# Kernel optimization log

Hardware: AMD Instinct MI355X
Metric: run time of the kernel (lower is better)

Reference implementation:

```python
import jax, jax.numpy as jnp
import numpy as np

EPS = 1e-5

def conv3(x, w, b):
    # 3x3 conv, stride 1, pad 1, NCHW/OIHW
    y = jax.lax.conv_general_dilated(x, w, (1, 1), ((1, 1), (1, 1)),
                                     dimension_numbers=('NCHW', 'OIHW', 'NCHW'))
    return y + b[None, :, None, None]

def positional_norm(x):
    # per-pixel channel-wise norm; torch .var() is unbiased (ddof=1)
    mean = jnp.mean(x, axis=1, keepdims=True)
    var = jnp.var(x, axis=1, keepdims=True, ddof=1)
    return (x - mean) / jnp.sqrt(var + EPS)

def bilinear_gather(x, py, px):
    # x: [B,C,H,W]; py/px: [B,K,H,W] absolute sample coords -> [B,C,K,H,W]
    B, C, H, W = x.shape
    K = py.shape[1]
    xf = x.reshape(B, C, H * W)
    y0 = jnp.floor(py).astype(jnp.int32)
    x0 = jnp.floor(px).astype(jnp.int32)
    wy = py - y0.astype(x.dtype)
    wx = px - x0.astype(x.dtype)

    def corner(yi, xi):
        valid = ((yi >= 0) & (yi < H) & (xi >= 0) & (xi < W)).astype(x.dtype)
        idx = (jnp.clip(yi, 0, H - 1) * W + jnp.clip(xi, 0, W - 1)).reshape(B, 1, K * H * W)
        v = jnp.take_along_axis(xf, idx, axis=2).reshape(B, C, K, H, W)
        return v * valid[:, None]

    out = ((1 - wy) * (1 - wx))[:, None] * corner(y0, x0)
    out = out + ((1 - wy) * wx)[:, None] * corner(y0, x0 + 1)
    out = out + (wy * (1 - wx))[:, None] * corner(y0 + 1, x0)
    out = out + (wy * wx)[:, None] * corner(y0 + 1, x0 + 1)
    return out

def dcn_v2(feat, cond, w_off, b_off, w_dcn, b_dcn):
    # DCNv2Pack: conv_offset(cond) -> (o1, o2, mask); modulated deformable 3x3 conv on feat
    B, C, H, W = feat.shape
    om = conv3(cond, w_off, b_off)                      # [B, 27, H, W]
    off = om[:, :18].reshape(B, 9, 2, H, W)             # (dy, dx) per kernel tap
    mask = jax.nn.sigmoid(om[:, 18:])                   # [B, 9, H, W]
    dy, dx = off[:, :, 0], off[:, :, 1]
    ki = jnp.repeat(jnp.arange(-1.0, 2.0, dtype=feat.dtype), 3)   # tap row offsets
    kj = jnp.tile(jnp.arange(-1.0, 2.0, dtype=feat.dtype), 3)     # tap col offsets
    hh = jnp.arange(H, dtype=feat.dtype)
    ww = jnp.arange(W, dtype=feat.dtype)
    py = dy + hh[None, None, :, None] + ki[None, :, None, None]
    px = dx + ww[None, None, None, :] + kj[None, :, None, None]
    sampled = bilinear_gather(feat, py, px)             # [B,C,9,H,W]
    wk = w_dcn.reshape(w_dcn.shape[0], C, 9)
    out = jnp.einsum('bkhw,bckhw,ock->bohw', mask, sampled, wk)
    return out + b_dcn[None, :, None, None]

def spade_forward(x, ref, w1, b1, w2, b2, w_off, b_off, w_dcn, b_dcn, w_g, b_g, w_be, b_be):
    normalized = positional_norm(x)
    h = jax.nn.relu(conv3(jnp.concatenate((normalized, ref), axis=1), w1, b1))
    cond = jax.nn.relu(conv3(h, w2, b2))
    ref_refine = dcn_v2(ref, cond, w_off, b_off, w_dcn, b_dcn)
    gamma = conv3(ref_refine, w_g, b_g)
    beta = conv3(ref_refine, w_be, b_be)
    return normalized * (1 + gamma) + beta

def setup_inputs() -> dict:
    key = jax.random.key(0)
    ks = jax.random.split(key, 16)
    B, NC, SC, H, W = 2, 64, 64, 96, 96
    mid = (NC + SC) // 8  # 16
    s = 0.05
    inp = {
        'x': jax.random.normal(ks[0], (B, NC, H, W), jnp.float32),
        'ref': jax.random.normal(ks[1], (B, SC, H, W), jnp.float32),
        'w1': jax.random.normal(ks[2], (mid, NC + SC, 3, 3), jnp.float32) * s,
        'b1': jax.random.normal(ks[3], (mid,), jnp.float32) * s,
        'w2': jax.random.normal(ks[4], (SC, mid, 3, 3), jnp.float32) * s,
        'b2': jax.random.normal(ks[5], (SC,), jnp.float32) * s,
        'w_off': jax.random.normal(ks[6], (27, SC, 3, 3), jnp.float32) * 0.01,
        'b_off': jax.random.normal(ks[7], (27,), jnp.float32) * 0.01,
        'w_dcn': jax.random.normal(ks[8], (SC, SC, 3, 3), jnp.float32) * s,
        'b_dcn': jax.random.normal(ks[9], (SC,), jnp.float32) * s,
        'w_g': jax.random.normal(ks[10], (NC, SC, 3, 3), jnp.float32) * s,
        'b_g': jax.random.normal(ks[11], (NC,), jnp.float32) * s,
        'w_be': jax.random.normal(ks[12], (NC, SC, 3, 3), jnp.float32) * s,
        'b_be': jax.random.normal(ks[13], (NC,), jnp.float32) * s,
    }
    return inp

def reference(x, ref, w1, b1, w2, b2, w_off, b_off, w_dcn, b_dcn, w_g, b_g, w_be, b_be):
    return spade_forward(x, ref, w1, b1, w2, b2, w_off, b_off, w_dcn, b_dcn, w_g, b_g, w_be, b_be)
```

## Files before the change

kernel.cpp:

```cpp
#include <hip/hip_runtime.h>
#include <math.h>

namespace {

typedef __attribute__((ext_vector_type(8))) short          bf16x8;
typedef __attribute__((ext_vector_type(8))) unsigned short u16x8;
typedef __attribute__((ext_vector_type(4))) float          f32x4;

constexpr int B_  = 2;
constexpr int H_  = 96;
constexpr int W_  = 96;
constexpr int HW_ = H_ * W_;
constexpr int NC_ = 64;
constexpr int SC_ = 64;

__device__ inline unsigned short f2bf(float f) {
    union { float f; unsigned u; } v; v.f = f;
    unsigned r = v.u + 0x7FFFu + ((v.u >> 16) & 1u);
    return (unsigned short)(r >> 16);
}
__device__ inline float bf2f(unsigned short s) {
    union { unsigned u; float f; } v; v.u = ((unsigned)s) << 16; return v.f;
}
__device__ inline bf16x8 ld_frag(const unsigned short* p) {
    return *reinterpret_cast<const bf16x8*>(p);
}

__global__ __launch_bounds__(256)
void prologue(const float* __restrict__ x, const float* __restrict__ ref,
              const float* __restrict__ w1, const float* __restrict__ w2,
              const float* __restrict__ woff, const float* __restrict__ wg,
              const float* __restrict__ wbe, const float* __restrict__ wdcn,
              float* __restrict__ nrm, unsigned short* __restrict__ cc,
              unsigned short* __restrict__ wt1, unsigned short* __restrict__ wt2,
              unsigned short* __restrict__ wtoff, unsigned short* __restrict__ wtg,
              unsigned short* __restrict__ wtbe, unsigned short* __restrict__ wbd) {
    __shared__ float red1[4][64];
    __shared__ float red2[4][64];
    __shared__ float rtile[64][65];

    int blk = blockIdx.x;
    int t   = threadIdx.x;

    if (blk < 288) {
        int b  = blk / 144;
        int p0 = (blk % 144) * 64;
        int px = t & 63;
        int cg = t >> 6;
        int p  = p0 + px;

        float v[16];
        float s1 = 0.f, s2 = 0.f;
        const float* xb = x + ((size_t)b * NC_ + cg * 16) * HW_ + p;
        #pragma unroll
        for (int j = 0; j < 16; ++j) {
            v[j] = xb[j * HW_];
            s1 += v[j];
            s2 = fmaf(v[j], v[j], s2);
        }
        red1[cg][px] = s1;
        red2[cg][px] = s2;

        const float* rb = ref + (size_t)b * SC_ * HW_ + p0 + px;
        #pragma unroll
        for (int it = 0; it < 16; ++it) {
            int ch = it * 4 + cg;
            rtile[ch][px] = rb[(size_t)ch * HW_];
        }
        __syncthreads();

        s1 = red1[0][px] + red1[1][px] + red1[2][px] + red1[3][px];
        s2 = red2[0][px] + red2[1][px] + red2[2][px] + red2[3][px];
        float mean = s1 * (1.f / 64.f);
        float var  = (s2 - 64.f * mean * mean) * (1.f / 63.f);
        float inv  = 1.f / sqrtf(var + 1e-5f);
        float* nb = nrm + ((size_t)b * NC_ + cg * 16) * HW_ + p;
        u16x8 pk[2];
        #pragma unroll
        for (int j = 0; j < 16; ++j) {
            float nv = (v[j] - mean) * inv;
            nb[j * HW_] = nv;
            pk[j >> 3][j & 7] = f2bf(nv);
        }
        size_t bp = (size_t)b * HW_ + p;
        *reinterpret_cast<u16x8*>(&cc[bp * 128 + cg * 16 + 0]) = pk[0];
        *reinterpret_cast<u16x8*>(&cc[bp * 128 + cg * 16 + 8]) = pk[1];

        {
            int wpx = t >> 2, q = t & 3;
            size_t bp2 = (size_t)b * HW_ + p0 + wpx;
            u16x8 o0, o1;
            #pragma unroll
            for (int j = 0; j < 8; ++j) {
                o0[j] = f2bf(rtile[q * 16 + j][wpx]);
                o1[j] = f2bf(rtile[q * 16 + 8 + j][wpx]);
            }
            *reinterpret_cast<u16x8*>(&cc[bp2 * 128 + 64 + q * 16 + 0]) = o0;
            *reinterpret_cast<u16x8*>(&cc[bp2 * 128 + 64 + q * 16 + 8]) = o1;
        }
    } else {
        int idx = (blk - 288) * 256 + t;
        if (idx < 9 * 16 * 128) {
            int tap = idx / (16 * 128), oc = (idx / 128) % 16, ic = idx % 128;
            wt1[idx] = f2bf(w1[(oc * 128 + ic) * 9 + tap]);
        }
        if (idx < 9 * 64 * 32) {
            int tap = idx / (64 * 32), oc = (idx / 32) % 64, ic = idx % 32;
            wt2[idx] = (ic < 16) ? f2bf(w2[(oc * 16 + ic) * 9 + tap]) : (unsigned short)0;
        }
        if (idx < 9 * 32 * 64) {
            int tap = idx / (32 * 64), oc = (idx / 64) % 32, ic = idx % 64;
            wtoff[idx] = (oc < 27) ? f2bf(woff[(oc * 64 + ic) * 9 + tap]) : (unsigned short)0;
        }
        if (idx < 9 * 64 * 64) {
            int tap = idx / (64 * 64), oc = (idx / 64) % 64, ic = idx % 64;
            wtg[idx]  = f2bf(wg [(oc * 64 + ic) * 9 + tap]);
            wtbe[idx] = f2bf(wbe[(oc * 64 + ic) * 9 + tap]);
        }
        if (idx < 64 * 576) {
            int oc = idx / 576, r = idx - oc * 576;
            int tap = r >> 6, ic = r & 63;
            wbd[idx] = f2bf(wdcn[oc * 576 + ic * 9 + tap]);
        }
    }
}

template <int ICS, int ICP, int COLP, int COUT_PAD, int COUT_REAL,
          bool DUAL, bool RELU, int OMODE>
__global__ __launch_bounds__(256)
void conv_bf(const unsigned short* __restrict__ in,
             const unsigned short* __restrict__ Wt,
             const unsigned short* __restrict__ Wt2,
             const float* __restrict__ bias, const float* __restrict__ bias2,
             const float* __restrict__ nrm, float* __restrict__ outF,
             unsigned short* __restrict__ outB) {
    constexpr int NOCT = COUT_PAD / 16;
    constexpr int WPO  = 4 / NOCT;
    constexpr int MTP  = NOCT;
    constexpr int NACC = DUAL ? 2 : 1;
    constexpr int NKS  = ICP / 32;
    constexpr int NCH8 = ICP / 8;

    __shared__ unsigned short patch[6 * 18 * COLP];

    int t   = threadIdx.x;
    int blk = blockIdx.x;
    int bx  = blk % 6;
    int by  = (blk / 6) % 24;
    int b   = blk / 144;
    int x0  = bx * 16, y0 = by * 4;

    for (int e = t; e < 6 * 18 * NCH8; e += 256) {
        int kc  = e % NCH8;
        int col = (e / NCH8) % 18;
        int row = e / (NCH8 * 18);
        int yy = y0 + row - 1, xx = x0 + col - 1;
        bf16x8 v = (bf16x8){0, 0, 0, 0, 0, 0, 0, 0};
        if (kc * 8 < ICS && (unsigned)yy < (unsigned)H_ && (unsigned)xx < (unsigned)W_) {
            v = ld_frag(&in[((size_t)b * HW_ + yy * W_ + xx) * ICS + kc * 8]);
        }
        *reinterpret_cast<bf16x8*>(&patch[(row * 18 + col) * COLP + kc * 8]) = v;
    }
    __syncthreads();

    int wave = t >> 6, lane = t & 63;
    int fr = lane & 15, fq = lane >> 4;
    int oct  = wave / WPO;
    int widx = wave - oct * WPO;
    int mt0  = widx * MTP;

    f32x4 acc[MTP][NACC];
    #pragma unroll
    for (int i = 0; i < MTP; ++i)
        #pragma unroll
        for (int a = 0; a < NACC; ++a)
            acc[i][a] = (f32x4){0.f, 0.f, 0.f, 0.f};

    constexpr int dyv[9] = {0,0,0,1,1,1,2,2,2};
    constexpr int dxv[9] = {0,1,2,0,1,2,0,1,2};

    #pragma unroll
    for (int tap = 0; tap < 9; ++tap) {
        int dy = dyv[tap], dx = dxv[tap];
        #pragma unroll
        for (int ks = 0; ks < NKS; ++ks) {
            const size_t wo = ((size_t)tap * COUT_PAD + oct * 16 + fr) * ICP + ks * 32 + fq * 8;
            bf16x8 wfA = ld_frag(&Wt[wo]);
            bf16x8 wfB;
            if (DUAL) wfB = ld_frag(&Wt2[wo]);
            #pragma unroll
            for (int i = 0; i < MTP; ++i) {
                bf16x8 pf = ld_frag(&patch[((mt0 + i + dy) * 18 + (fr + dx)) * COLP
                                           + ks * 32 + fq * 8]);
                acc[i][0] = __builtin_amdgcn_mfma_f32_16x16x32_bf16(wfA, pf, acc[i][0], 0, 0, 0);
                if (DUAL)
                    acc[i][1] = __builtin_amdgcn_mfma_f32_16x16x32_bf16(wfB, pf, acc[i][1], 0, 0, 0);
            }
        }
    }

    #pragma unroll
    for (int i = 0; i < MTP; ++i) {
        int py = mt0 + i;
        if (OMODE == 1) {
            size_t p = (size_t)b * HW_ + (size_t)(y0 + py) * W_ + x0 + fr;
            ushort4 sv;
            #pragma unroll
            for (int j = 0; j < 4; ++j) {
                float v = acc[i][0][j] + bias[oct * 16 + fq * 4 + j];
                if (RELU) v = fmaxf(v, 0.f);
                ((unsigned short*)&sv)[j] = f2bf(v);
            }
            *reinterpret_cast<ushort4*>(&outB[p * COUT_REAL + oct * 16 + fq * 4]) = sv;
        } else if (OMODE == 2) {
            size_t p = (size_t)b * HW_ + (size_t)(y0 + py) * W_ + x0 + fr;
            float4 o4;
            #pragma unroll
            for (int j = 0; j < 4; ++j) {
                int oc = oct * 16 + fq * 4 + j;
                float v = acc[i][0][j] + (oc < COUT_REAL ? bias[oc] : 0.f);
                ((float*)&o4)[j] = v;
            }
            *reinterpret_cast<float4*>(&outF[p * 32 + oct * 16 + fq * 4]) = o4;
        } else {
            #pragma unroll
            for (int j = 0; j < 4; ++j) {
                int oc = oct * 16 + fq * 4 + j;
                if (oc >= COUT_REAL) continue;
                size_t off = ((size_t)b * COUT_REAL + oc) * HW_
                           + (size_t)(y0 + py) * W_ + x0 + fr;
                float v = acc[i][0][j] + bias[oc];
                if (DUAL) {
                    float be = acc[i][1][j] + bias2[oc];
                    float nv = nrm[off];
                    outF[off] = fmaf(nv, 1.f + v, be);
                } else {
                    outF[off] = RELU ? fmaxf(v, 0.f) : v;
                }
            }
        }
    }
}

constexpr int SROW = 584;
constexpr int DT   = 32;

__global__ __launch_bounds__(256)
void dcn_kernel(const unsigned short* __restrict__ cc, const float* __restrict__ omP,
                const unsigned short* __restrict__ wbd, const float* __restrict__ b_dcn,
                unsigned short* __restrict__ rrT) {
    __shared__ unsigned short sS[DT * SROW];
    __shared__ float4 cwL[DT * 9];
    __shared__ int4   ciL[DT * 9];

    int t = threadIdx.x;
    int bid = blockIdx.x;
    int swz = (bid & 7) * 72 + (bid >> 3);
    int b   = swz / (HW_ / DT);
    int p0  = (swz % (HW_ / DT)) * DT;

    const unsigned short* ccb = cc + (size_t)b * HW_ * 128;

    for (int e = t; e < DT * 9; e += 256) {
        int pp = e / 9, k = e - pp * 9;
        int p  = p0 + pp;
        int y  = p / W_, x = p - y * W_;
        const float* omp = &omP[(size_t)(b * HW_ + p) * 32];
        float dy = omp[2 * k];
        float dx = omp[2 * k + 1];
        float mk = omp[18 + k];
        mk = 1.f / (1.f + expf(-mk));

        float py = dy + (float)y + (float)(k / 3 - 1);
        float px = dx + (float)x + (float)(k % 3 - 1);
        float fy = floorf(py), fx = floorf(px);
        int   y0 = (int)fy,   x0 = (int)fx;
        float wy = py - fy,   wx = px - fx;

        float cw[4];
        int   ci[4];
        #pragma unroll
        for (int i = 0; i < 4; ++i) {
            int yy = y0 + (i >> 1);
            int xx = x0 + (i & 1);
            bool valid = (yy >= 0) && (yy < H_) && (xx >= 0) && (xx < W_);
            int yc = yy < 0 ? 0 : (yy > H_ - 1 ? H_ - 1 : yy);
            int xc = xx < 0 ? 0 : (xx > W_ - 1 ? W_ - 1 : xx);
            ci[i] = yc * W_ + xc;
            float wyi = (i >> 1) ? wy : (1.f - wy);
            float wxi = (i & 1)  ? wx : (1.f - wx);
            cw[i] = valid ? mk * wyi * wxi : 0.f;
        }
        cwL[e] = make_float4(cw[0], cw[1], cw[2], cw[3]);
        ciL[e] = make_int4(ci[0], ci[1], ci[2], ci[3]);
    }
    __syncthreads();

    {
        int pp = t >> 3, cg8 = t & 7;
        #pragma unroll
        for (int k = 0; k < 9; ++k) {
            float4 cw = cwL[pp * 9 + k];
            int4   ci = ciL[pp * 9 + k];
            u16x8 r0 = *reinterpret_cast<const u16x8*>(&ccb[(size_t)ci.x * 128 + 64 + cg8 * 8]);
            u16x8 r1 = *reinterpret_cast<const u16x8*>(&ccb[(size_t)ci.y * 128 + 64 + cg8 * 8]);
            u16x8 r2 = *reinterpret_cast<const u16x8*>(&ccb[(size_t)ci.z * 128 + 64 + cg8 * 8]);
            u16x8 r3 = *reinterpret_cast<const u16x8*>(&ccb[(size_t)ci.w * 128 + 64 + cg8 * 8]);
            u16x8 sv;
            #pragma unroll
            for (int j = 0; j < 8; ++j) {
                float v = cw.x * bf2f(r0[j]) + cw.y * bf2f(r1[j])
                        + cw.z * bf2f(r2[j]) + cw.w * bf2f(r3[j]);
                sv[j] = f2bf(v);
            }
            *reinterpret_cast<u16x8*>(&sS[pp * SROW + k * 64 + cg8 * 8]) = sv;
        }
    }
    __syncthreads();

    int wave = t >> 6, lane = t & 63;
    int fr = lane & 15, fq = lane >> 4;

    f32x4 acc0 = (f32x4){0.f, 0.f, 0.f, 0.f};
    f32x4 acc1 = (f32x4){0.f, 0.f, 0.f, 0.f};
    for (int ks = 0; ks < 18; ++ks) {
        bf16x8 wf  = ld_frag(&wbd[(size_t)(wave * 16 + fr) * 576 + ks * 32 + fq * 8]);
        bf16x8 pf0 = ld_frag(&sS[(size_t)fr * SROW + ks * 32 + fq * 8]);
        bf16x8 pf1 = ld_frag(&sS[(size_t)(16 + fr) * SROW + ks * 32 + fq * 8]);
        acc0 = __builtin_amdgcn_mfma_f32_16x16x32_bf16(wf, pf0, acc0, 0, 0, 0);
        acc1 = __builtin_amdgcn_mfma_f32_16x16x32_bf16(wf, pf1, acc1, 0, 0, 0);
    }

    {
        size_t p = (size_t)b * HW_ + p0 + fr;
        ushort4 sv0, sv1;
        #pragma unroll
        for (int j = 0; j < 4; ++j) {
            float bo = b_dcn[wave * 16 + fq * 4 + j];
            ((unsigned short*)&sv0)[j] = f2bf(acc0[j] + bo);
            ((unsigned short*)&sv1)[j] = f2bf(acc1[j] + bo);
        }
        *reinterpret_cast<ushort4*>(&rrT[p * 64 + wave * 16 + fq * 4]) = sv0;
        *reinterpret_cast<ushort4*>(&rrT[(p + 16) * 64 + wave * 16 + fq * 4]) = sv1;
    }
}

}

extern "C" void kernel_launch(void* const* d_in, const int* in_sizes, int n_in,
                              void* d_out, int out_size, void* d_ws, size_t ws_size,
                              hipStream_t stream) {
    (void)in_sizes; (void)n_in; (void)out_size; (void)ws_size;

    const float* x     = (const float*)d_in[0];
    const float* ref   = (const float*)d_in[1];
    const float* w1    = (const float*)d_in[2];
    const float* b1    = (const float*)d_in[3];
    const float* w2    = (const float*)d_in[4];
    const float* b2    = (const float*)d_in[5];
    const float* w_off = (const float*)d_in[6];
    const float* b_off = (const float*)d_in[7];
    const float* w_dcn = (const float*)d_in[8];
    const float* b_dcn = (const float*)d_in[9];
    const float* w_g   = (const float*)d_in[10];
    const float* b_g   = (const float*)d_in[11];
    const float* w_be  = (const float*)d_in[12];
    const float* b_be  = (const float*)d_in[13];

    float* out = (float*)d_out;
    float* ws  = (float*)d_ws;

    float* nrm = ws;
    float* omP = nrm + 1179648;
    unsigned short* cc    = (unsigned short*)(omP + 589824);
    unsigned short* hmidT = cc    + 2359296;
    unsigned short* condT = hmidT + 294912;
    unsigned short* rrT   = condT + 1179648;
    unsigned short* wt1   = rrT   + 1179648;
    unsigned short* wt2   = wt1   + 18432;
    unsigned short* wtoff = wt2   + 18432;
    unsigned short* wtg   = wtoff + 18432;
    unsigned short* wtbe  = wtg   + 36864;
    unsigned short* wbd   = wtbe  + 36864;

    prologue<<<432, 256, 0, stream>>>(x, ref, w1, w2, w_off, w_g, w_be, w_dcn,
                                      nrm, cc, wt1, wt2, wtoff, wtg, wtbe, wbd);

    constexpr int GRID = 288;

    conv_bf<128, 128, 136, 16, 16, false, true, 1>
        <<<GRID, 256, 0, stream>>>(cc, wt1, nullptr, b1, nullptr, nullptr, nullptr, hmidT);

    conv_bf<16, 32, 40, 64, 64, false, true, 1>
        <<<GRID, 256, 0, stream>>>(hmidT, wt2, nullptr, b2, nullptr, nullptr, nullptr, condT);

    conv_bf<64, 64, 72, 32, 27, false, false, 2>
        <<<GRID, 256, 0, stream>>>(condT, wtoff, nullptr, b_off, nullptr, nullptr, omP, nullptr);

    dcn_kernel<<<B_ * (HW_ / DT), 256, 0, stream>>>(cc, omP, wbd, b_dcn, rrT);

    conv_bf<64, 64, 72, 64, 64, true, false, 0>
        <<<GRID, 256, 0, stream>>>(rrT, wtg, wtbe, b_g, b_be, nrm, out, nullptr);
}
```

Baseline: 68.44 us.

## Fuse offset conv into DCN kernel and switch bilinear sampling to fp16

The separate offset/mask conv launch and its fp32 workspace round trip are removed. Each DCN block now loads a 3x34 halo of condT into shared memory and computes its 27 offset channels with MFMA before sampling. The bilinear gather also reads a new compact fp16 copy of ref (64 channels per pixel instead of a 128-wide interleaved buffer), blends with packed fp16 math, and the DCN GEMM uses fp16 MFMA. This saves a launch and memory traffic but adds per-block conv work, extra prologue writes, and fp16 range/precision risk.

New measurement: 68.02 us. No clear change (-0.6%).

```diff
diff --git a/kernel.cpp b/kernel.cpp
--- a/kernel.cpp
+++ b/kernel.cpp
@@ -5,6 +5,7 @@
 
 typedef __attribute__((ext_vector_type(8))) short          bf16x8;
 typedef __attribute__((ext_vector_type(8))) unsigned short u16x8;
+typedef __attribute__((ext_vector_type(8))) _Float16       f16x8;
 typedef __attribute__((ext_vector_type(4))) float          f32x4;
 
 constexpr int B_  = 2;
@@ -19,8 +20,11 @@
     unsigned r = v.u + 0x7FFFu + ((v.u >> 16) & 1u);
     return (unsigned short)(r >> 16);
 }
-__device__ inline float bf2f(unsigned short s) {
-    union { unsigned u; float f; } v; v.u = ((unsigned)s) << 16; return v.f;
+__device__ inline unsigned short f2hbits(float f) {
+    union { _Float16 h; unsigned short u; } s; s.h = (_Float16)f; return s.u;
+}
+__device__ inline _Float16 hfrombits(unsigned short u) {
+    union { _Float16 h; unsigned short u; } s; s.u = u; return s.h;
 }
 __device__ inline bf16x8 ld_frag(const unsigned short* p) {
     return *reinterpret_cast<const bf16x8*>(p);
@@ -32,9 +36,10 @@
               const float* __restrict__ woff, const float* __restrict__ wg,
               const float* __restrict__ wbe, const float* __restrict__ wdcn,
               float* __restrict__ nrm, unsigned short* __restrict__ cc,
+              unsigned short* __restrict__ ccH,
               unsigned short* __restrict__ wt1, unsigned short* __restrict__ wt2,
               unsigned short* __restrict__ wtoff, unsigned short* __restrict__ wtg,
-              unsigned short* __restrict__ wtbe, unsigned short* __restrict__ wbd) {
+              unsigned short* __restrict__ wtbe, unsigned short* __restrict__ wbdH) {
     __shared__ float red1[4][64];
     __shared__ float red2[4][64];
     __shared__ float rtile[64][65];
@@ -89,14 +94,18 @@
         {
             int wpx = t >> 2, q = t & 3;
             size_t bp2 = (size_t)b * HW_ + p0 + wpx;
-            u16x8 o0, o1;
+            u16x8 o0, o1, h0, h1;
             #pragma unroll
             for (int j = 0; j < 8; ++j) {
-                o0[j] = f2bf(rtile[q * 16 + j][wpx]);
-                o1[j] = f2bf(rtile[q * 16 + 8 + j][wpx]);
+                float v0 = rtile[q * 16 + j][wpx];
+                float v1 = rtile[q * 16 + 8 + j][wpx];
+                o0[j] = f2bf(v0);    o1[j] = f2bf(v1);
+                h0[j] = f2hbits(v0); h1[j] = f2hbits(v1);
             }
             *reinterpret_cast<u16x8*>(&cc[bp2 * 128 + 64 + q * 16 + 0]) = o0;
             *reinterpret_cast<u16x8*>(&cc[bp2 * 128 + 64 + q * 16 + 8]) = o1;
+            *reinterpret_cast<u16x8*>(&ccH[bp2 * 64 + q * 16 + 0]) = h0;
+            *reinterpret_cast<u16x8*>(&ccH[bp2 * 64 + q * 16 + 8]) = h1;
         }
     } else {
         int idx = (blk - 288) * 256 + t;
@@ -120,7 +129,7 @@
         if (idx < 64 * 576) {
             int oc = idx / 576, r = idx - oc * 576;
             int tap = r >> 6, ic = r & 63;
-            wbd[idx] = f2bf(wdcn[oc * 576 + ic * 9 + tap]);
+            wbdH[idx] = f2hbits(wdcn[oc * 576 + ic * 9 + tap]);
         }
     }
 }
@@ -212,16 +221,6 @@
                 ((unsigned short*)&sv)[j] = f2bf(v);
             }
             *reinterpret_cast<ushort4*>(&outB[p * COUT_REAL + oct * 16 + fq * 4]) = sv;
-        } else if (OMODE == 2) {
-            size_t p = (size_t)b * HW_ + (size_t)(y0 + py) * W_ + x0 + fr;
-            float4 o4;
-            #pragma unroll
-            for (int j = 0; j < 4; ++j) {
-                int oc = oct * 16 + fq * 4 + j;
-                float v = acc[i][0][j] + (oc < COUT_REAL ? bias[oc] : 0.f);
-                ((float*)&o4)[j] = v;
-            }
-            *reinterpret_cast<float4*>(&outF[p * 32 + oct * 16 + fq * 4]) = o4;
         } else {
             #pragma unroll
             for (int j = 0; j < 4; ++j) {
@@ -246,89 +245,138 @@
 constexpr int DT   = 32;
 
 __global__ __launch_bounds__(256)
-void dcn_kernel(const unsigned short* __restrict__ cc, const float* __restrict__ omP,
-                const unsigned short* __restrict__ wbd, const float* __restrict__ b_dcn,
+void dcn_kernel(const unsigned short* __restrict__ ccH,
+                const unsigned short* __restrict__ condT,
+                const unsigned short* __restrict__ wtoff,
+                const float* __restrict__ b_off,
+                const unsigned short* __restrict__ wbdH,
+                const float* __restrict__ b_dcn,
                 unsigned short* __restrict__ rrT) {
-    __shared__ unsigned short sS[DT * SROW];
-    __shared__ float4 cwL[DT * 9];
-    __shared__ int4   ciL[DT * 9];
+    __shared__ unsigned short uS[DT * SROW];
+    __shared__ float  omL[DT][36];
+    __shared__ ushort4 cwLh[DT * 9];
+    __shared__ int4    ciL[DT * 9];
 
     int t = threadIdx.x;
     int bid = blockIdx.x;
     int swz = (bid & 7) * 72 + (bid >> 3);
     int b   = swz / (HW_ / DT);
     int p0  = (swz % (HW_ / DT)) * DT;
-
-    const unsigned short* ccb = cc + (size_t)b * HW_ * 128;
+    int y   = p0 / W_, x0 = p0 - y * W_;
+
+    for (int e = t; e < 3 * 34 * 8; e += 256) {
+        int kc  = e & 7;
+        int col = (e >> 3) % 34;
+        int row = (e >> 3) / 34;
+        int yy = y + row - 1, xx = x0 + col - 1;
+        bf16x8 v = (bf16x8){0, 0, 0, 0, 0, 0, 0, 0};
+        if ((unsigned)yy < (unsigned)H_ && (unsigned)xx < (unsigned)W_) {
+            v = ld_frag(&condT[((size_t)b * HW_ + yy * W_ + xx) * 64 + kc * 8]);
+        }
+        *reinterpret_cast<bf16x8*>(&uS[(row * 34 + col) * 72 + kc * 8]) = v;
+    }
+    __syncthreads();
+
+    int wave = t >> 6, lane = t & 63;
+    int fr = lane & 15, fq = lane >> 4;
+
+    {
+        int oct = wave & 1, mt = wave >> 1;
+        f32x4 acc = (f32x4){0.f, 0.f, 0.f, 0.f};
+        constexpr int dyv[9] = {0,0,0,1,1,1,2,2,2};
+        constexpr int dxv[9] = {0,1,2,0,1,2,0,1,2};
+        #pragma unroll
+        for (int tap = 0; tap < 9; ++tap) {
+            int dy = dyv[tap], dx = dxv[tap];
+            #pragma unroll
+            for (int ks = 0; ks < 2; ++ks) {
+                bf16x8 wf = ld_frag(&wtoff[((size_t)tap * 32 + oct * 16 + fr) * 64
+                                           + ks * 32 + fq * 8]);
+                bf16x8 pf = *reinterpret_cast<const bf16x8*>(
+                    &uS[(dy * 34 + mt * 16 + fr + dx) * 72 + ks * 32 + fq * 8]);
+                acc = __builtin_amdgcn_mfma_f32_16x16x32_bf16(wf, pf, acc, 0, 0, 0);
+            }
+        }
+        int px = mt * 16 + fr;
+        float4 o4;
+        #pragma unroll
+        for (int j = 0; j < 4; ++j) {
+            int oc = oct * 16 + fq * 4 + j;
+            ((float*)&o4)[j] = acc[j] + (oc < 27 ? b_off[oc] : 0.f);
+        }
+        *reinterpret_cast<float4*>(&omL[px][oct * 16 + fq * 4]) = o4;
+    }
+    __syncthreads();
 
     for (int e = t; e < DT * 9; e += 256) {
         int pp = e / 9, k = e - pp * 9;
         int p  = p0 + pp;
-        int y  = p / W_, x = p - y * W_;
-        const float* omp = &omP[(size_t)(b * HW_ + p) * 32];
-        float dy = omp[2 * k];
-        float dx = omp[2 * k + 1];
-        float mk = omp[18 + k];
+        int yq = p / W_, xq = p - yq * W_;
+        float dy = omL[pp][2 * k];
+        float dx = omL[pp][2 * k + 1];
+        float mk = omL[pp][18 + k];
         mk = 1.f / (1.f + expf(-mk));
 
-        float py = dy + (float)y + (float)(k / 3 - 1);
-        float px = dx + (float)x + (float)(k % 3 - 1);
+        float py = dy + (float)yq + (float)(k / 3 - 1);
+        float px = dx + (float)xq + (float)(k % 3 - 1);
         float fy = floorf(py), fx = floorf(px);
-        int   y0 = (int)fy,   x0 = (int)fx;
+        int   y0 = (int)fy,   x0c = (int)fx;
         float wy = py - fy,   wx = px - fx;
 
-        float cw[4];
+        ushort4 cwh;
         int   ci[4];
         #pragma unroll
         for (int i = 0; i < 4; ++i) {
             int yy = y0 + (i >> 1);
-            int xx = x0 + (i & 1);
+            int xx = x0c + (i & 1);
             bool valid = (yy >= 0) && (yy < H_) && (xx >= 0) && (xx < W_);
             int yc = yy < 0 ? 0 : (yy > H_ - 1 ? H_ - 1 : yy);
             int xc = xx < 0 ? 0 : (xx > W_ - 1 ? W_ - 1 : xx);
             ci[i] = yc * W_ + xc;
             float wyi = (i >> 1) ? wy : (1.f - wy);
             float wxi = (i & 1)  ? wx : (1.f - wx);
-            cw[i] = valid ? mk * wyi * wxi : 0.f;
-        }
-        cwL[e] = make_float4(cw[0], cw[1], cw[2], cw[3]);
+            ((unsigned short*)&cwh)[i] = f2hbits(valid ? mk * wyi * wxi : 0.f);
+        }
+        cwLh[e] = cwh;
         ciL[e] = make_int4(ci[0], ci[1], ci[2], ci[3]);
     }
     __syncthreads();
 
     {
+        const unsigned short* ch = ccH + (size_t)b * HW_ * 64;
         int pp = t >> 3, cg8 = t & 7;
         #pragma unroll
         for (int k = 0; k < 9; ++k) {
-            float4 cw = cwL[pp * 9 + k];
-            int4   ci = ciL[pp * 9 + k];
-            u16x8 r0 = *reinterpret_cast<const u16x8*>(&ccb[(size_t)ci.x * 128 + 64 + cg8 * 8]);
-            u16x8 r1 = *reinterpret_cast<const u16x8*>(&ccb[(size_t)ci.y * 128 + 64 + cg8 * 8]);
-            u16x8 r2 = *reinterpret_cast<const u16x8*>(&ccb[(size_t)ci.z * 128 + 64 + cg8 * 8]);
-            u16x8 r3 = *reinterpret_cast<const u16x8*>(&ccb[(size_t)ci.w * 128 + 64 + cg8 * 8]);
-            u16x8 sv;
-            #pragma unroll
-            for (int j = 0; j < 8; ++j) {
-                float v = cw.x * bf2f(r0[j]) + cw.y * bf2f(r1[j])
-                        + cw.z * bf2f(r2[j]) + cw.w * bf2f(r3[j]);
-                sv[j] = f2bf(v);
-            }
-            *reinterpret_cast<u16x8*>(&sS[pp * SROW + k * 64 + cg8 * 8]) = sv;
+            ushort4 cwh = cwLh[pp * 9 + k];
+            int4    ci  = ciL[pp * 9 + k];
+            f16x8 r0 = *reinterpret_cast<const f16x8*>(&ch[(size_t)ci.x * 64 + cg8 * 8]);
+            f16x8 r1 = *reinterpret_cast<const f16x8*>(&ch[(size_t)ci.y * 64 + cg8 * 8]);
+            f16x8 r2 = *reinterpret_cast<const f16x8*>(&ch[(size_t)ci.z * 64 + cg8 * 8]);
+            f16x8 r3 = *reinterpret_cast<const f16x8*>(&ch[(size_t)ci.w * 64 + cg8 * 8]);
+            _Float16 h0 = hfrombits(cwh.x);
+            _Float16 h1 = hfrombits(cwh.y);
+            _Float16 h2 = hfrombits(cwh.z);
+            _Float16 h3 = hfrombits(cwh.w);
+            f16x8 s = r0 * h0;
+            s += r1 * h1;
+            s += r2 * h2;
+            s += r3 * h3;
+            *reinterpret_cast<f16x8*>(&uS[pp * SROW + k * 64 + cg8 * 8]) = s;
         }
     }
     __syncthreads();
-
-    int wave = t >> 6, lane = t & 63;
-    int fr = lane & 15, fq = lane >> 4;
 
     f32x4 acc0 = (f32x4){0.f, 0.f, 0.f, 0.f};
     f32x4 acc1 = (f32x4){0.f, 0.f, 0.f, 0.f};
     for (int ks = 0; ks < 18; ++ks) {
-        bf16x8 wf  = ld_frag(&wbd[(size_t)(wave * 16 + fr) * 576 + ks * 32 + fq * 8]);
-        bf16x8 pf0 = ld_frag(&sS[(size_t)fr * SROW + ks * 32 + fq * 8]);
-        bf16x8 pf1 = ld_frag(&sS[(size_t)(16 + fr) * SROW + ks * 32 + fq * 8]);
-        acc0 = __builtin_amdgcn_mfma_f32_16x16x32_bf16(wf, pf0, acc0, 0, 0, 0);
-        acc1 = __builtin_amdgcn_mfma_f32_16x16x32_bf16(wf, pf1, acc1, 0, 0, 0);
+        f16x8 wf  = *reinterpret_cast<const f16x8*>(
+            &wbdH[(size_t)(wave * 16 + fr) * 576 + ks * 32 + fq * 8]);
+        f16x8 pf0 = *reinterpret_cast<const f16x8*>(
+            &uS[(size_t)fr * SROW + ks * 32 + fq * 8]);
+        f16x8 pf1 = *reinterpret_cast<const f16x8*>(
+            &uS[(size_t)(16 + fr) * SROW + ks * 32 + fq * 8]);
+        acc0 = __builtin_amdgcn_mfma_f32_16x16x32_f16(wf, pf0, acc0, 0, 0, 0);
+        acc1 = __builtin_amdgcn_mfma_f32_16x16x32_f16(wf, pf1, acc1, 0, 0, 0);
     }
 
     {
@@ -371,9 +419,9 @@
     float* ws  = (float*)d_ws;
 
     float* nrm = ws;
-    float* omP = nrm + 1179648;
-    unsigned short* cc    = (unsigned short*)(omP + 589824);
-    unsigned short* hmidT = cc    + 2359296;
+    unsigned short* cc    = (unsigned short*)(nrm + 1179648);
+    unsigned short* ccH   = cc    + 2359296;
+    unsigned short* hmidT = ccH   + 1179648;
     unsigned short* condT = hmidT + 294912;
     unsigned short* rrT   = condT + 1179648;
     unsigned short* wt1   = rrT   + 1179648;
@@ -381,10 +429,10 @@
     unsigned short* wtoff = wt2   + 18432;
     unsigned short* wtg   = wtoff + 18432;
     unsigned short* wtbe  = wtg   + 36864;
-    unsigned short* wbd   = wtbe  + 36864;
+    unsigned short* wbdH  = wtbe  + 36864;
 
     prologue<<<432, 256, 0, stream>>>(x, ref, w1, w2, w_off, w_g, w_be, w_dcn,
-                                      nrm, cc, wt1, wt2, wtoff, wtg, wtbe, wbd);
+                                      nrm, cc, ccH, wt1, wt2, wtoff, wtg, wtbe, wbdH);
 
     constexpr int GRID = 288;
 
@@ -394,10 +442,8 @@
     conv_bf<16, 32, 40, 64, 64, false, true, 1>
         <<<GRID, 256, 0, stream>>>(hmidT, wt2, nullptr, b2, nullptr, nullptr, nullptr, condT);
 
-    conv_bf<64, 64, 72, 32, 27, false, false, 2>
-        <<<GRID, 256, 0, stream>>>(condT, wtoff, nullptr, b_off, nullptr, nullptr, omP, nullptr);
-
-    dcn_kernel<<<B_ * (HW_ / DT), 256, 0, stream>>>(cc, omP, wbd, b_dcn, rrT);
+    dcn_kernel<<<B_ * (HW_ / DT), 256, 0, stream>>>(ccH, condT, wtoff, b_off,
+                                                    wbdH, b_dcn, rrT);
 
     conv_bf<64, 64, 72, 64, 64, true, false, 0>
         <<<GRID, 256, 0, stream>>>(rrT, wtg, wtbe, b_g, b_be, nrm, out, nullptr);
```
